# Kernel tuning notes

Measured on AMD Instinct MI355X. Metric: run time of the kernel, lower is better.

The kernel has to match this reference:

```python
import jax, jax.numpy as jnp
import numpy as np

D_MODEL = 1024
NUM_HEADS = 16
D_K = D_MODEL // NUM_HEADS
B, L = 2, 2048
NEG = -1e9


def setup_inputs() -> dict:
    key = jax.random.key(0)
    ks = jax.random.split(key, 11)
    s = 1.0 / np.sqrt(D_MODEL)
    inp = {
        "Q": jax.random.normal(ks[0], (B, L, D_MODEL), jnp.float32),
        "K": jax.random.normal(ks[1], (B, L, D_MODEL), jnp.float32),
        "V": jax.random.normal(ks[2], (B, L, D_MODEL), jnp.float32),
        # causal mask: True = valid (attend), False = masked
        "mask": jnp.tril(jnp.ones((L, L), bool))[None, None],
        # torch nn.Linear weights stored [out, in]
        "Wq": jax.random.normal(ks[3], (D_MODEL, D_MODEL), jnp.float32) * s,
        "bq": jnp.zeros((D_MODEL,), jnp.float32),
        "Wk": jax.random.normal(ks[4], (D_MODEL, D_MODEL), jnp.float32) * s,
        "bk": jnp.zeros((D_MODEL,), jnp.float32),
        "Wv": jax.random.normal(ks[5], (D_MODEL, D_MODEL), jnp.float32) * s,
        "bv": jnp.zeros((D_MODEL,), jnp.float32),
        "Wo": jax.random.normal(ks[6], (D_MODEL, D_MODEL), jnp.float32) * s,
        "bo": jnp.zeros((D_MODEL,), jnp.float32),
    }
    return inp


def _split_heads(x):  # [B,L,D] -> [B,H,L,d_k]
    b, l, _ = x.shape
    return x.reshape(b, l, NUM_HEADS, D_K).transpose(0, 2, 1, 3)


def reference(Q, K, V, mask, Wq, bq, Wk, bk, Wv, bv, Wo, bo):
    # linear projections (torch Linear: x @ W.T + b)
    q = _split_heads(Q @ Wq.T + bq)
    k = _split_heads(K @ Wk.T + bk)
    v = _split_heads(V @ Wv.T + bv)
    scores = jnp.einsum("bhqd,bhkd->bhqk", q, k) / jnp.sqrt(jnp.float32(D_K))
    scores = jnp.where(mask, scores, NEG)
    probs = jax.nn.softmax(scores, axis=-1)  # dropout inactive at inference
    attn = jnp.einsum("bhqk,bhkd->bhqd", probs, v)
    b, h, l, dk = attn.shape
    o_in = attn.transpose(0, 2, 1, 3).reshape(b, l, D_MODEL)
    return o_in @ Wo.T + bo
```

## Files before the change

kernel.cpp:

```cpp
#include <hip/hip_runtime.h>
#include <stdint.h>

#define D_MODEL 1024
#define NH 16
#define DK 64
#define BBATCH 2
#define LL 2048
#define SCALE_LOG2E 0.1803368801111244f

typedef unsigned short bfu;
typedef __attribute__((ext_vector_type(8))) short bf16x8;
typedef __attribute__((ext_vector_type(4))) float f32x4;

union BF8 { uint32_t w[4]; bf16x8 v; };

__device__ __forceinline__ bfu f2bf(float f) {
    union { float f; uint32_t u; } a; a.f = f;
    uint32_t r = a.u + 0x7FFF + ((a.u >> 16) & 1);
    return (bfu)(r >> 16);
}
__device__ __forceinline__ uint32_t pktrunc(float hi, float lo) {
    return __builtin_amdgcn_perm(__float_as_uint(hi), __float_as_uint(lo), 0x07060302);
}

__device__ __forceinline__ void gload_lds16(const void* g, void* l) {
    __builtin_amdgcn_global_load_lds(
        (const __attribute__((address_space(1))) void*)g,
        (__attribute__((address_space(3))) void*)l, 16, 0, 0);
}

__device__ __forceinline__ int swz(int R, int G) {
    return R * 64 + (((G ^ (R & 7))) << 3);
}

__global__ __launch_bounds__(256) void cvt_all(
    const float4* __restrict__ s0, const float4* __restrict__ s1, const float4* __restrict__ s2,
    const float4* __restrict__ s3, const float4* __restrict__ s4, const float4* __restrict__ s5,
    const float4* __restrict__ s6, ushort4* __restrict__ dst)
{
    int i = blockIdx.x * 256 + threadIdx.x;
    const float4* s; int off;
    float sc = 1.0f;
    if (i < (3 << 20)) {
        int t = i >> 20; s = (t == 0) ? s0 : ((t == 1) ? s1 : s2);
        off = i & ((1 << 20) - 1);
    } else {
        int j = i - (3 << 20);
        int t = j >> 18; s = (t == 0) ? s3 : ((t == 1) ? s4 : ((t == 2) ? s5 : s6));
        if (t == 0) sc = SCALE_LOG2E;
        off = j & ((1 << 18) - 1);
    }
    float4 v = s[off];
    ushort4 o;
    o.x = f2bf(v.x * sc); o.y = f2bf(v.y * sc); o.z = f2bf(v.z * sc); o.w = f2bf(v.w * sc);
    dst[i] = o;
}

#define BM 128
#define BN 128
#define BKK 64

__device__ __forceinline__ int kperm(int k) {
    return (((k >> 4) & 1) << 5) | (((k >> 2) & 3) << 3) | (((k >> 5) & 1) << 2) | (k & 3);
}

__global__ __launch_bounds__(256, 2) void gemm_proj(
    const bfu* __restrict__ Qb, const bfu* __restrict__ Kb, const bfu* __restrict__ Vb,
    const bfu* __restrict__ Wq, const bfu* __restrict__ Wk, const bfu* __restrict__ Wv,
    const float* __restrict__ bq, const float* __restrict__ bk, const float* __restrict__ bv,
    bfu* __restrict__ qp, bfu* __restrict__ kp, bfu* __restrict__ vt)
{
    const int z = blockIdx.z;
    const bfu* A = (z == 0) ? Qb : ((z == 1) ? Kb : Vb);
    const bfu* B = (z == 0) ? Wq : ((z == 1) ? Wk : Wv);
    const float* bias = (z == 0) ? bq : ((z == 1) ? bk : bv);
    const float bsc = (z == 0) ? SCALE_LOG2E : 1.0f;
    bfu* out = (z == 0) ? qp : ((z == 1) ? kp : vt);

    __shared__ __align__(16) bfu As[BM * BKK];
    __shared__ __align__(16) bfu Bs[BN * BKK];

    const int t = threadIdx.x;
    const int lane = t & 63;
    const int wave = t >> 6;
    const int wm = wave & 1, wn = wave >> 1;
    const int tm = blockIdx.y * BM, tn = blockIdx.x * BN;
    const int lr = lane & 15, quad = lane >> 4;

    f32x4 acc[4][4];
    for (int i = 0; i < 4; i++) for (int j = 0; j < 4; j++) acc[i][j] = (f32x4){0.f, 0.f, 0.f, 0.f};

    for (int kt = 0; kt < 1024; kt += BKK) {
        for (int it = 0; it < 4; ++it) {
            int c = t + it * 256;
            int row = c >> 3, gx = (c & 7) ^ (row & 7);
            gload_lds16(&A[(size_t)(tm + row) * 1024 + kt + gx * 8], &As[(size_t)c * 8]);
        }
        for (int it = 0; it < 4; ++it) {
            int c = t + it * 256;
            int row = c >> 3, gx = (c & 7) ^ (row & 7);
            gload_lds16(&B[(size_t)(tn + row) * 1024 + kt + gx * 8], &Bs[(size_t)c * 8]);
        }
        __syncthreads();
        for (int kx = 0; kx < 2; kx++) {
            bf16x8 a[4], b[4];
            for (int i = 0; i < 4; i++)
                a[i] = *(const bf16x8*)&As[swz(wm * 64 + i * 16 + lr, kx * 4 + quad)];
            for (int i = 0; i < 4; i++)
                b[i] = *(const bf16x8*)&Bs[swz(wn * 64 + i * 16 + lr, kx * 4 + quad)];
            for (int mt = 0; mt < 4; mt++)
                for (int nt = 0; nt < 4; nt++)
                    acc[mt][nt] = __builtin_amdgcn_mfma_f32_16x16x32_bf16(a[mt], b[nt], acc[mt][nt], 0, 0, 0);
        }
        __syncthreads();
    }

    for (int mt = 0; mt < 4; mt++)
        for (int nt = 0; nt < 4; nt++)
            for (int r = 0; r < 4; r++) {
                int m = tm + wm * 64 + mt * 16 + quad * 4 + r;
                int n = tn + wn * 64 + nt * 16 + lr;
                float v = acc[mt][nt][r] + bias[n] * bsc;
                int b_ = m >> 11, l = m & 2047;
                int h = n >> 6, d = n & 63;
                if (z < 2)
                    out[((size_t)((b_ * NH + h) * LL + l)) * DK + d] = f2bf(v);
                else {
                    int lp = (l & ~63) | kperm(l & 63);
                    out[((size_t)((b_ * NH + h) * DK + d)) * LL + lp] = f2bf(v);
                }
            }
}

__global__ __launch_bounds__(128, 4) void attn_kernel(
    const bfu* __restrict__ qp, const bfu* __restrict__ kp, const bfu* __restrict__ vtp,
    bfu* __restrict__ attn)
{
    const int id = blockIdx.x;
    const int bh = (id & 7) | (((id >> 3) & 3) << 3);
    const int band = 31 - (id >> 5);
    const int b_ = bh >> 4, h = bh & 15;
    const int t = threadIdx.x;
    const int lane = t & 63, w = t >> 6;
    const int lr = lane & 15, quad = lane >> 4, q8 = quad << 3;

    __shared__ __align__(16) bfu Ks[2][64 * 64];
    __shared__ __align__(16) bfu Vs[2][64 * 64];

    const int r0 = band * 64 + w * 32;
    const int jmax = band;

    const bfu* kbase = kp + (size_t)bh * LL * DK;
    const bfu* vbase = vtp + (size_t)bh * DK * LL;

    bf16x8 aq[2][2];
    for (int mt = 0; mt < 2; mt++)
        for (int kx = 0; kx < 2; kx++)
            aq[mt][kx] = *(const bf16x8*)&qp[((size_t)bh * LL + r0 + mt * 16 + lr) * DK + kx * 32 + q8];

    f32x4 o[2][4];
    for (int mt = 0; mt < 2; mt++)
        for (int nf = 0; nf < 4; nf++) o[mt][nf] = (f32x4){0.f, 0.f, 0.f, 0.f};
    float lsum[2] = {0.f, 0.f};

    for (int it = 0; it < 4; ++it) {
        int c = t + it * 128;
        int r = c >> 3, gx = (c & 7) ^ (r & 7);
        gload_lds16(&kbase[(size_t)r * DK + gx * 8], &Ks[0][(size_t)c * 8]);
        gload_lds16(&vbase[(size_t)r * LL + gx * 8], &Vs[0][(size_t)c * 8]);
    }
    __syncthreads();

    for (int j = 0; j <= jmax; ++j) {
        const int buf = j & 1;
        if (j < jmax) {
            const int nb = buf ^ 1, jn = j + 1;
            for (int it = 0; it < 4; ++it) {
                int c = t + it * 128;
                int r = c >> 3, gx = (c & 7) ^ (r & 7);
                gload_lds16(&kbase[(size_t)(jn * 64 + r) * DK + gx * 8], &Ks[nb][(size_t)c * 8]);
                gload_lds16(&vbase[(size_t)r * LL + jn * 64 + gx * 8], &Vs[nb][(size_t)c * 8]);
            }
        }
        f32x4 sv[4][2];
        for (int kt = 0; kt < 4; kt++)
            for (int mt = 0; mt < 2; mt++) sv[kt][mt] = (f32x4){0.f, 0.f, 0.f, 0.f};
        for (int kx = 0; kx < 2; kx++)
            for (int kt = 0; kt < 4; kt++) {
                bf16x8 ak = *(const bf16x8*)&Ks[buf][swz(kt * 16 + lr, kx * 4 + quad)];
                for (int mt = 0; mt < 2; mt++)
                    sv[kt][mt] = __builtin_amdgcn_mfma_f32_16x16x32_bf16(ak, aq[mt][kx], sv[kt][mt], 0, 0, 0);
            }
        if (j == jmax) {
            const int mb = r0 & 63;
            for (int kt = 0; kt < 4; kt++)
                for (int mt = 0; mt < 2; mt++)
                    for (int r = 0; r < 4; r++) {
                        int kl = kt * 16 + quad * 4 + r;
                        int ml = mb + mt * 16 + lr;
                        if (kl > ml) sv[kt][mt][r] = -1e9f;
                    }
        }
        for (int kt = 0; kt < 4; kt++)
            for (int mt = 0; mt < 2; mt++)
                for (int r = 0; r < 4; r++) {
                    float e = __builtin_amdgcn_exp2f(sv[kt][mt][r]);
                    sv[kt][mt][r] = e;
                    lsum[mt] += e;
                }
        for (int kx = 0; kx < 2; kx++) {
            BF8 pf[2];
            for (int mt = 0; mt < 2; mt++) {
                pf[mt].w[0] = pktrunc(sv[kx][mt][1], sv[kx][mt][0]);
                pf[mt].w[1] = pktrunc(sv[kx][mt][3], sv[kx][mt][2]);
                pf[mt].w[2] = pktrunc(sv[2 + kx][mt][1], sv[2 + kx][mt][0]);
                pf[mt].w[3] = pktrunc(sv[2 + kx][mt][3], sv[2 + kx][mt][2]);
            }
            for (int nf = 0; nf < 4; nf++) {
                bf16x8 av = *(const bf16x8*)&Vs[buf][swz(nf * 16 + lr, kx * 4 + quad)];
                for (int mt = 0; mt < 2; mt++)
                    o[mt][nf] = __builtin_amdgcn_mfma_f32_16x16x32_bf16(av, pf[mt].v, o[mt][nf], 0, 0, 0);
            }
        }
        __syncthreads();
    }

    for (int mt = 0; mt < 2; mt++) {
        float l = lsum[mt];
        l += __shfl_xor(l, 16);
        l += __shfl_xor(l, 32);
        float rinv = 1.0f / l;
        for (int nf = 0; nf < 4; nf++) {
            uint32_t w0 = ((uint32_t)f2bf(o[mt][nf][1] * rinv) << 16) | f2bf(o[mt][nf][0] * rinv);
            uint32_t w1 = ((uint32_t)f2bf(o[mt][nf][3] * rinv) << 16) | f2bf(o[mt][nf][2] * rinv);
            uint2 pk2 = {w0, w1};
            *(uint2*)&attn[((size_t)(b_ * LL + r0 + mt * 16 + lr)) * D_MODEL + h * DK + nf * 16 + quad * 4] = pk2;
        }
    }
}

#define OBM 128
#define OBN 64

__global__ __launch_bounds__(256) void gemm_out(
    const bfu* __restrict__ A, const bfu* __restrict__ B,
    const float* __restrict__ bias, float* __restrict__ out)
{
    __shared__ __align__(16) bfu As[OBM * 64];
    __shared__ __align__(16) bfu Bs[OBN * 64];

    const int t = threadIdx.x;
    const int lane = t & 63, w = t >> 6;
    const int tm = blockIdx.y * OBM, tn = blockIdx.x * OBN;
    const int lr = lane & 15, quad = lane >> 4;

    f32x4 acc[2][4];
    for (int i = 0; i < 2; i++) for (int j = 0; j < 4; j++) acc[i][j] = (f32x4){0.f, 0.f, 0.f, 0.f};

    for (int kt = 0; kt < 1024; kt += 64) {
        for (int it = 0; it < 4; ++it) {
            int c = t + it * 256;
            int row = c >> 3, gx = (c & 7) ^ (row & 7);
            gload_lds16(&A[(size_t)(tm + row) * 1024 + kt + gx * 8], &As[(size_t)c * 8]);
        }
        for (int it = 0; it < 2; ++it) {
            int c = t + it * 256;
            int row = c >> 3, gx = (c & 7) ^ (row & 7);
            gload_lds16(&B[(size_t)(tn + row) * 1024 + kt + gx * 8], &Bs[(size_t)c * 8]);
        }
        __syncthreads();
        for (int kx = 0; kx < 2; kx++) {
            bf16x8 a[2], b[4];
            for (int mt = 0; mt < 2; mt++)
                a[mt] = *(const bf16x8*)&As[swz(w * 32 + mt * 16 + lr, kx * 4 + quad)];
            for (int nt = 0; nt < 4; nt++)
                b[nt] = *(const bf16x8*)&Bs[swz(nt * 16 + lr, kx * 4 + quad)];
            for (int mt = 0; mt < 2; mt++)
                for (int nt = 0; nt < 4; nt++)
                    acc[mt][nt] = __builtin_amdgcn_mfma_f32_16x16x32_bf16(a[mt], b[nt], acc[mt][nt], 0, 0, 0);
        }
        __syncthreads();
    }

    for (int mt = 0; mt < 2; mt++)
        for (int nt = 0; nt < 4; nt++)
            for (int r = 0; r < 4; r++) {
                int m = tm + w * 32 + mt * 16 + quad * 4 + r;
                int n = tn + nt * 16 + lr;
                out[(size_t)m * D_MODEL + n] = acc[mt][nt][r] + bias[n];
            }
}

extern "C" void kernel_launch(void* const* d_in, const int* in_sizes, int n_in,
                              void* d_out, int out_size, void* d_ws, size_t ws_size,
                              hipStream_t stream) {
    const float* Q  = (const float*)d_in[0];
    const float* K  = (const float*)d_in[1];
    const float* V  = (const float*)d_in[2];
    const float* Wq = (const float*)d_in[4];
    const float* bq = (const float*)d_in[5];
    const float* Wk = (const float*)d_in[6];
    const float* bk = (const float*)d_in[7];
    const float* Wv = (const float*)d_in[8];
    const float* bv = (const float*)d_in[9];
    const float* Wo = (const float*)d_in[10];
    const float* bo = (const float*)d_in[11];
    float* out = (float*)d_out;

    char* ws = (char*)d_ws;
    bfu* Qb  = (bfu*)(ws + ((size_t)0  << 20));
    bfu* Kb  = (bfu*)(ws + ((size_t)8  << 20));
    bfu* Vb  = (bfu*)(ws + ((size_t)16 << 20));
    bfu* Wqb = (bfu*)(ws + ((size_t)24 << 20));
    bfu* Wkb = (bfu*)(ws + ((size_t)26 << 20));
    bfu* Wvb = (bfu*)(ws + ((size_t)28 << 20));
    bfu* Wob = (bfu*)(ws + ((size_t)30 << 20));
    bfu* qp  = (bfu*)(ws + ((size_t)32 << 20));
    bfu* kp  = (bfu*)(ws + ((size_t)40 << 20));
    bfu* vt  = (bfu*)(ws + ((size_t)48 << 20));
    bfu* attn = (bfu*)(ws + ((size_t)56 << 20));

    cvt_all<<<16384, 256, 0, stream>>>(
        (const float4*)Q, (const float4*)K, (const float4*)V,
        (const float4*)Wq, (const float4*)Wk, (const float4*)Wv, (const float4*)Wo,
        (ushort4*)Qb);

    gemm_proj<<<dim3(8, 32, 3), 256, 0, stream>>>(Qb, Kb, Vb, Wqb, Wkb, Wvb,
                                                  bq, bk, bv, qp, kp, vt);

    attn_kernel<<<dim3(1024), 128, 0, stream>>>(qp, kp, vt, attn);

    gemm_out<<<dim3(16, 32), 256, 0, stream>>>(attn, Wob, bo, out);
}
```

Before: 232.3 us.

## Split attention KV loop across two wave pairs and merge partial sums in LDS

Each attention block now has 256 threads. Two wave pairs cover the same 64 query rows, and each pair processes half of the causal KV tiles with its own double-buffered LDS staging. The partial outputs and row sums are then combined through LDS before normalization and the store. This shortens the serial KV loop of long-band blocks, which should reduce the tail imbalance from causal masking. In exchange it doubles LDS per block, adds a reduction step, and still syncs the whole block each iteration. No max subtraction is used, so adding the unnormalized sums stays valid.

```diff
diff --git a/kernel.cpp b/kernel.cpp
--- a/kernel.cpp
+++ b/kernel.cpp
@@ -132,7 +132,7 @@
             }
 }
 
-__global__ __launch_bounds__(128, 4) void attn_kernel(
+__global__ __launch_bounds__(256, 2) void attn_kernel(
     const bfu* __restrict__ qp, const bfu* __restrict__ kp, const bfu* __restrict__ vtp,
     bfu* __restrict__ attn)
 {
@@ -142,13 +142,20 @@
     const int b_ = bh >> 4, h = bh & 15;
     const int t = threadIdx.x;
     const int lane = t & 63, w = t >> 6;
+    const int hw = w & 1;
+    const int jh = w >> 1;
     const int lr = lane & 15, quad = lane >> 4, q8 = quad << 3;
 
-    __shared__ __align__(16) bfu Ks[2][64 * 64];
-    __shared__ __align__(16) bfu Vs[2][64 * 64];
-
-    const int r0 = band * 64 + w * 32;
-    const int jmax = band;
+    __shared__ __align__(16) bfu Ks[2][2][64 * 64];
+    __shared__ __align__(16) bfu Vs[2][2][64 * 64];
+
+    const int n  = band + 1;
+    const int n0 = (n + 1) >> 1;
+    const int nj = (jh == 0) ? n0 : (n - n0);
+    const int jb = (jh == 0) ? 0 : n0;
+
+    const int tl = t & 127;
+    const int r0 = band * 64 + hw * 32;
 
     const bfu* kbase = kp + (size_t)bh * LL * DK;
     const bfu* vbase = vtp + (size_t)bh * DK * LL;
@@ -163,78 +170,108 @@
         for (int nf = 0; nf < 4; nf++) o[mt][nf] = (f32x4){0.f, 0.f, 0.f, 0.f};
     float lsum[2] = {0.f, 0.f};
 
-    for (int it = 0; it < 4; ++it) {
-        int c = t + it * 128;
-        int r = c >> 3, gx = (c & 7) ^ (r & 7);
-        gload_lds16(&kbase[(size_t)r * DK + gx * 8], &Ks[0][(size_t)c * 8]);
-        gload_lds16(&vbase[(size_t)r * LL + gx * 8], &Vs[0][(size_t)c * 8]);
+    if (nj > 0) {
+        for (int it = 0; it < 4; ++it) {
+            int c = tl + it * 128;
+            int r = c >> 3, gx = (c & 7) ^ (r & 7);
+            gload_lds16(&kbase[(size_t)(jb * 64 + r) * DK + gx * 8], &Ks[jh][0][(size_t)c * 8]);
+            gload_lds16(&vbase[(size_t)r * LL + jb * 64 + gx * 8], &Vs[jh][0][(size_t)c * 8]);
+        }
     }
     __syncthreads();
 
-    for (int j = 0; j <= jmax; ++j) {
-        const int buf = j & 1;
-        if (j < jmax) {
-            const int nb = buf ^ 1, jn = j + 1;
+    for (int i = 0; i < n0; ++i) {
+        const int buf = i & 1;
+        if (i + 1 < nj) {
+            const int nb = buf ^ 1, jn = jb + i + 1;
             for (int it = 0; it < 4; ++it) {
-                int c = t + it * 128;
+                int c = tl + it * 128;
                 int r = c >> 3, gx = (c & 7) ^ (r & 7);
-                gload_lds16(&kbase[(size_t)(jn * 64 + r) * DK + gx * 8], &Ks[nb][(size_t)c * 8]);
-                gload_lds16(&vbase[(size_t)r * LL + jn * 64 + gx * 8], &Vs[nb][(size_t)c * 8]);
-            }
-        }
-        f32x4 sv[4][2];
-        for (int kt = 0; kt < 4; kt++)
-            for (int mt = 0; mt < 2; mt++) sv[kt][mt] = (f32x4){0.f, 0.f, 0.f, 0.f};
-        for (int kx = 0; kx < 2; kx++)
-            for (int kt = 0; kt < 4; kt++) {
-                bf16x8 ak = *(const bf16x8*)&Ks[buf][swz(kt * 16 + lr, kx * 4 + quad)];
-                for (int mt = 0; mt < 2; mt++)
-                    sv[kt][mt] = __builtin_amdgcn_mfma_f32_16x16x32_bf16(ak, aq[mt][kx], sv[kt][mt], 0, 0, 0);
-            }
-        if (j == jmax) {
-            const int mb = r0 & 63;
+                gload_lds16(&kbase[(size_t)(jn * 64 + r) * DK + gx * 8], &Ks[jh][nb][(size_t)c * 8]);
+                gload_lds16(&vbase[(size_t)r * LL + jn * 64 + gx * 8], &Vs[jh][nb][(size_t)c * 8]);
+            }
+        }
+        if (i < nj) {
+            const int j = jb + i;
+            const bfu* Kt = Ks[jh][buf];
+            const bfu* Vt = Vs[jh][buf];
+            f32x4 sv[4][2];
+            for (int kt = 0; kt < 4; kt++)
+                for (int mt = 0; mt < 2; mt++) sv[kt][mt] = (f32x4){0.f, 0.f, 0.f, 0.f};
+            for (int kx = 0; kx < 2; kx++)
+                for (int kt = 0; kt < 4; kt++) {
+                    bf16x8 ak = *(const bf16x8*)&Kt[swz(kt * 16 + lr, kx * 4 + quad)];
+                    for (int mt = 0; mt < 2; mt++)
+                        sv[kt][mt] = __builtin_amdgcn_mfma_f32_16x16x32_bf16(ak, aq[mt][kx], sv[kt][mt], 0, 0, 0);
+                }
+            if (j == band) {
+                const int mb = r0 & 63;
+                for (int kt = 0; kt < 4; kt++)
+                    for (int mt = 0; mt < 2; mt++)
+                        for (int r = 0; r < 4; r++) {
+                            int kl = kt * 16 + quad * 4 + r;
+                            int ml = mb + mt * 16 + lr;
+                            if (kl > ml) sv[kt][mt][r] = -1e9f;
+                        }
+            }
             for (int kt = 0; kt < 4; kt++)
                 for (int mt = 0; mt < 2; mt++)
                     for (int r = 0; r < 4; r++) {
-                        int kl = kt * 16 + quad * 4 + r;
-                        int ml = mb + mt * 16 + lr;
-                        if (kl > ml) sv[kt][mt][r] = -1e9f;
+                        float e = __builtin_amdgcn_exp2f(sv[kt][mt][r]);
+                        sv[kt][mt][r] = e;
+                        lsum[mt] += e;
                     }
-        }
-        for (int kt = 0; kt < 4; kt++)
-            for (int mt = 0; mt < 2; mt++)
-                for (int r = 0; r < 4; r++) {
-                    float e = __builtin_amdgcn_exp2f(sv[kt][mt][r]);
-                    sv[kt][mt][r] = e;
-                    lsum[mt] += e;
+            for (int kx = 0; kx < 2; kx++) {
+                BF8 pf[2];
+                for (int mt = 0; mt < 2; mt++) {
+                    pf[mt].w[0] = pktrunc(sv[kx][mt][1], sv[kx][mt][0]);
+                    pf[mt].w[1] = pktrunc(sv[kx][mt][3], sv[kx][mt][2]);
+                    pf[mt].w[2] = pktrunc(sv[2 + kx][mt][1], sv[2 + kx][mt][0]);
+                    pf[mt].w[3] = pktrunc(sv[2 + kx][mt][3], sv[2 + kx][mt][2]);
                 }
-        for (int kx = 0; kx < 2; kx++) {
-            BF8 pf[2];
-            for (int mt = 0; mt < 2; mt++) {
-                pf[mt].w[0] = pktrunc(sv[kx][mt][1], sv[kx][mt][0]);
-                pf[mt].w[1] = pktrunc(sv[kx][mt][3], sv[kx][mt][2]);
-                pf[mt].w[2] = pktrunc(sv[2 + kx][mt][1], sv[2 + kx][mt][0]);
-                pf[mt].w[3] = pktrunc(sv[2 + kx][mt][3], sv[2 + kx][mt][2]);
-            }
+                for (int nf = 0; nf < 4; nf++) {
+                    bf16x8 av = *(const bf16x8*)&Vt[swz(nf * 16 + lr, kx * 4 + quad)];
+                    for (int mt = 0; mt < 2; mt++)
+                        o[mt][nf] = __builtin_amdgcn_mfma_f32_16x16x32_bf16(av, pf[mt].v, o[mt][nf], 0, 0, 0);
+                }
+            }
+        }
+        __syncthreads();
+    }
+
+    float* Of = (float*)&Ks[0][0][0];
+    float* Lf = (float*)&Vs[0][0][0];
+    const int ci = hw * 64 + lane;
+    if (jh == 1) {
+        float* dst = Of + ci * 33;
+        for (int mt = 0; mt < 2; mt++)
+            for (int nf = 0; nf < 4; nf++)
+                for (int r = 0; r < 4; r++)
+                    dst[mt * 16 + nf * 4 + r] = o[mt][nf][r];
+        Lf[ci * 2 + 0] = lsum[0];
+        Lf[ci * 2 + 1] = lsum[1];
+    }
+    __syncthreads();
+    if (jh == 0) {
+        const float* src = Of + ci * 33;
+        for (int mt = 0; mt < 2; mt++)
+            for (int nf = 0; nf < 4; nf++)
+                for (int r = 0; r < 4; r++)
+                    o[mt][nf][r] += src[mt * 16 + nf * 4 + r];
+        lsum[0] += Lf[ci * 2 + 0];
+        lsum[1] += Lf[ci * 2 + 1];
+
+        for (int mt = 0; mt < 2; mt++) {
+            float l = lsum[mt];
+            l += __shfl_xor(l, 16);
+            l += __shfl_xor(l, 32);
+            float rinv = 1.0f / l;
             for (int nf = 0; nf < 4; nf++) {
-                bf16x8 av = *(const bf16x8*)&Vs[buf][swz(nf * 16 + lr, kx * 4 + quad)];
-                for (int mt = 0; mt < 2; mt++)
-                    o[mt][nf] = __builtin_amdgcn_mfma_f32_16x16x32_bf16(av, pf[mt].v, o[mt][nf], 0, 0, 0);
-            }
-        }
-        __syncthreads();
-    }
-
-    for (int mt = 0; mt < 2; mt++) {
-        float l = lsum[mt];
-        l += __shfl_xor(l, 16);
-        l += __shfl_xor(l, 32);
-        float rinv = 1.0f / l;
-        for (int nf = 0; nf < 4; nf++) {
-            uint32_t w0 = ((uint32_t)f2bf(o[mt][nf][1] * rinv) << 16) | f2bf(o[mt][nf][0] * rinv);
-            uint32_t w1 = ((uint32_t)f2bf(o[mt][nf][3] * rinv) << 16) | f2bf(o[mt][nf][2] * rinv);
-            uint2 pk2 = {w0, w1};
-            *(uint2*)&attn[((size_t)(b_ * LL + r0 + mt * 16 + lr)) * D_MODEL + h * DK + nf * 16 + quad * 4] = pk2;
+                uint32_t w0 = ((uint32_t)f2bf(o[mt][nf][1] * rinv) << 16) | f2bf(o[mt][nf][0] * rinv);
+                uint32_t w1 = ((uint32_t)f2bf(o[mt][nf][3] * rinv) << 16) | f2bf(o[mt][nf][2] * rinv);
+                uint2 pk2 = {w0, w1};
+                *(uint2*)&attn[((size_t)(b_ * LL + r0 + mt * 16 + lr)) * D_MODEL + h * DK + nf * 16 + quad * 4] = pk2;
+            }
         }
     }
 }
@@ -328,7 +365,7 @@
     gemm_proj<<<dim3(8, 32, 3), 256, 0, stream>>>(Qb, Kb, Vb, Wqb, Wkb, Wvb,
                                                   bq, bk, bv, qp, kp, vt);
 
-    attn_kernel<<<dim3(1024), 128, 0, stream>>>(qp, kp, vt, attn);
+    attn_kernel<<<dim3(1024), 256, 0, stream>>>(qp, kp, vt, attn);
 
     gemm_out<<<dim3(16, 32), 256, 0, stream>>>(attn, Wob, bo, out);
 }
```

New measurement: 218.9 us. -5.8%, faster.
